# Kernel tuning notes

Measured on AMD Instinct MI355X. Metric: run time of the kernel, lower is better.

Reference implementation:

```python
import jax, jax.numpy as jnp
import numpy as np

D_MODEL = 1024
N_HEADS = 16
HEAD_DIM = D_MODEL // N_HEADS
FF_DIM = 1024  # repo bug: linear2 is Linear(d_model, ff_dim); ff_dim==d_model required for residual
EPS = 1e-5


def _linear_params(k, d_in, d_out):
    kw, kb = jax.random.split(k)
    bound = 1.0 / np.sqrt(d_in)
    W = jax.random.uniform(kw, (d_out, d_in), minval=-bound, maxval=bound, dtype=jnp.float32)
    b = jax.random.uniform(kb, (d_out,), minval=-bound, maxval=bound, dtype=jnp.float32)
    return W, b


def setup_inputs() -> dict:
    key = jax.random.key(0)
    ks = jax.random.split(key, 8)
    src = jax.random.normal(ks[0], (4, 2048, D_MODEL), dtype=jnp.float32)
    Wq, bq = _linear_params(ks[1], D_MODEL, D_MODEL)
    Wk, bk = _linear_params(ks[2], D_MODEL, D_MODEL)
    Wv, bv = _linear_params(ks[3], D_MODEL, D_MODEL)
    Wo, bo = _linear_params(ks[4], D_MODEL, D_MODEL)
    W1, b1 = _linear_params(ks[5], D_MODEL, FF_DIM)
    W2, b2 = _linear_params(ks[6], D_MODEL, FF_DIM)
    g1 = jnp.ones((D_MODEL,), jnp.float32); be1 = jnp.zeros((D_MODEL,), jnp.float32)
    g2 = jnp.ones((D_MODEL,), jnp.float32); be2 = jnp.zeros((D_MODEL,), jnp.float32)
    return {"src": src, "Wq": Wq, "bq": bq, "Wk": Wk, "bk": bk, "Wv": Wv, "bv": bv,
            "Wo": Wo, "bo": bo, "W1": W1, "b1": b1, "W2": W2, "b2": b2,
            "g1": g1, "be1": be1, "g2": g2, "be2": be2}


def _layernorm(x, g, b):
    mu = jnp.mean(x, axis=-1, keepdims=True)
    var = jnp.var(x, axis=-1, keepdims=True)
    return (x - mu) * jax.lax.rsqrt(var + EPS) * g + b


def _mha(x, Wq, bq, Wk, bk, Wv, bv, Wo, bo):
    B, S, _ = x.shape
    def proj(W, b):
        return (x @ W.T + b).reshape(B, S, N_HEADS, HEAD_DIM).transpose(0, 2, 1, 3)
    Q, K, V = proj(Wq, bq), proj(Wk, bk), proj(Wv, bv)
    scale = jnp.float32(np.sqrt(HEAD_DIM))
    energy = jnp.einsum('bhqd,bhkd->bhqk', Q, K) / scale
    attn = jax.nn.softmax(energy, axis=-1)
    out = jnp.einsum('bhqk,bhkd->bhqd', attn, V)
    out = out.transpose(0, 2, 1, 3).reshape(B, S, D_MODEL)
    return out @ Wo.T + bo


def reference(src, Wq, bq, Wk, bk, Wv, bv, Wo, bo, W1, b1, W2, b2, g1, be1, g2, be2):
    x = src
    x = x + _mha(_layernorm(x, g1, be1), Wq, bq, Wk, bk, Wv, bv, Wo, bo)
    h = _layernorm(x, g2, be2)
    ff = jax.nn.relu(h @ W1.T + b1) @ W2.T + b2
    return x + ff
```

## Files before the change

### kernel.cpp

```cpp
#include <hip/hip_runtime.h>
#include <stdint.h>

typedef __attribute__((ext_vector_type(8))) short    bf16x8;
typedef __attribute__((ext_vector_type(4))) short    bf16x4;
typedef __attribute__((ext_vector_type(4))) float    f32x4;
typedef __attribute__((ext_vector_type(8))) uint16_t u16x8;
typedef __attribute__((ext_vector_type(4))) uint16_t u16x4;

#define D_MODEL 1024
#define SEQ     2048
#define NB      4
#define NH      16
#define HD      64
#define MTOK    8192

__device__ __forceinline__ float bf2f(uint16_t u) {
    union { uint32_t i; float f; } x; x.i = ((uint32_t)u) << 16; return x.f;
}
__device__ __forceinline__ uint16_t f2bf(float f) {
    union { float f; uint32_t i; } x; x.f = f;
    uint32_t r = (x.i + 0x7fffu + ((x.i >> 16) & 1u)) >> 16;
    return (uint16_t)r;
}
__device__ __forceinline__ void gload16(const void* g, void* l) {
    __builtin_amdgcn_global_load_lds(
        (const __attribute__((address_space(1))) unsigned int*)g,
        (__attribute__((address_space(3))) unsigned int*)l, 16, 0, 0);
}
__device__ __forceinline__ bf16x8 lds_ld8(const uint16_t* p) {
    bf16x4 a = *(const bf16x4*)p;
    bf16x4 b = *(const bf16x4*)(p + 4);
    bf16x8 r;
    r[0] = a[0]; r[1] = a[1]; r[2] = a[2]; r[3] = a[3];
    r[4] = b[0]; r[5] = b[1]; r[6] = b[2]; r[7] = b[3];
    return r;
}
__device__ __forceinline__ uint32_t pk_bf16_trunc(float lo, float hi) {
    return __builtin_amdgcn_perm(__float_as_uint(hi), __float_as_uint(lo), 0x07060302u);
}

__global__ __launch_bounds__(256)
void cvt_all(const float* __restrict__ s0, const float* __restrict__ s1,
             const float* __restrict__ s2, const float* __restrict__ s3,
             const float* __restrict__ s4, const float* __restrict__ s5,
             uint16_t* __restrict__ dQKV, uint16_t* __restrict__ dWo,
             uint16_t* __restrict__ dW1, uint16_t* __restrict__ dW2)
{
    const float* srcs[6] = {s0, s1, s2, s3, s4, s5};
    uint16_t* dsts[6] = {dQKV, dQKV + (size_t)D_MODEL * D_MODEL,
                         dQKV + 2 * (size_t)D_MODEL * D_MODEL, dWo, dW1, dW2};
    const float* in = srcs[blockIdx.y];
    uint16_t* out = dsts[blockIdx.y];
    const int i = (blockIdx.x * 256 + threadIdx.x) * 4;
    float4 v = *(const float4*)(in + i);
    u16x4 o;
    o[0] = f2bf(v.x); o[1] = f2bf(v.y); o[2] = f2bf(v.z); o[3] = f2bf(v.w);
    *(u16x4*)(out + i) = o;
}

__global__ __launch_bounds__(256)
void ln_kernel(const float* __restrict__ x, const float* __restrict__ g,
               const float* __restrict__ be, uint16_t* __restrict__ y)
{
    const int row = blockIdx.x;
    const int tid = threadIdx.x;
    const size_t base = (size_t)row * D_MODEL + tid * 4;
    float4 v = *(const float4*)(x + base);
    float f[4] = {v.x, v.y, v.z, v.w};
    float sum = 0.f, sq = 0.f;
#pragma unroll
    for (int e = 0; e < 4; e++) { sum += f[e]; sq += f[e] * f[e]; }
#pragma unroll
    for (int o = 32; o > 0; o >>= 1) { sum += __shfl_down(sum, o); sq += __shfl_down(sq, o); }
    __shared__ float ps[4], pq[4];
    const int lane = tid & 63, wid = tid >> 6;
    if (lane == 0) { ps[wid] = sum; pq[wid] = sq; }
    __syncthreads();
    const float ts = ps[0] + ps[1] + ps[2] + ps[3];
    const float tq = pq[0] + pq[1] + pq[2] + pq[3];
    const float mean = ts * (1.0f / D_MODEL);
    const float var  = tq * (1.0f / D_MODEL) - mean * mean;
    const float rstd = rsqrtf(var + 1e-5f);
    float4 gv = *(const float4*)(g + tid * 4);
    float4 bv = *(const float4*)(be + tid * 4);
    const float gg[4] = {gv.x, gv.y, gv.z, gv.w};
    const float bb[4] = {bv.x, bv.y, bv.z, bv.w};
    u16x4 outv;
#pragma unroll
    for (int e = 0; e < 4; e++)
        outv[e] = f2bf((f[e] - mean) * rstd * gg[e] + bb[e]);
    *(u16x4*)(y + base) = outv;
}

template<int RESID, int RELU, int OUTF32>
__global__ __launch_bounds__(256, 4)
void gemm_bt64(const uint16_t* __restrict__ A, const uint16_t* __restrict__ W,
               const float* __restrict__ bias, const float* __restrict__ resid,
               void* __restrict__ Cv)
{
    __shared__ uint16_t lA[64 * 32];
    __shared__ uint16_t lB[128 * 32];
    const int tid  = threadIdx.x;
    const int lane = tid & 63;
    const int quad = lane >> 4;
    const int l16  = lane & 15;
    const int wid  = tid >> 6;
    const int wm   = wid >> 1;
    const int wn   = wid & 1;
    const int m0   = blockIdx.y * 64;
    const int n0   = blockIdx.x * 128;

    f32x4 acc[2][4];
#pragma unroll
    for (int i = 0; i < 2; i++)
#pragma unroll
        for (int j = 0; j < 4; j++) acc[i][j] = (f32x4){0.f, 0.f, 0.f, 0.f};

    const int sr = tid >> 2;
    const int sc = (tid & 3) * 8;
    const uint16_t* gA0 = A + (size_t)(m0 + sr) * D_MODEL + sc;
    const uint16_t* gW0 = W + (size_t)(n0 + sr) * D_MODEL + sc;
    const uint16_t* gW1 = gW0 + (size_t)64 * D_MODEL;
    uint16_t* sA0 = &lA[tid * 8];
    uint16_t* sB0 = &lB[tid * 8];
    uint16_t* sB1 = sB0 + 2048;

    for (int k0 = 0; k0 < D_MODEL; k0 += 32) {
        __syncthreads();
        gload16(gA0 + k0, sA0);
        gload16(gW0 + k0, sB0);
        gload16(gW1 + k0, sB1);
        __syncthreads();
        bf16x8 af[2], bfr[4];
#pragma unroll
        for (int i = 0; i < 2; i++)
            af[i] = *(const bf16x8*)&lA[(wm * 32 + i * 16 + l16) * 32 + quad * 8];
#pragma unroll
        for (int j = 0; j < 4; j++)
            bfr[j] = *(const bf16x8*)&lB[(wn * 64 + j * 16 + l16) * 32 + quad * 8];
#pragma unroll
        for (int i = 0; i < 2; i++)
#pragma unroll
            for (int j = 0; j < 4; j++)
                acc[i][j] = __builtin_amdgcn_mfma_f32_16x16x32_bf16(af[i], bfr[j], acc[i][j], 0, 0, 0);
    }

#pragma unroll
    for (int j = 0; j < 4; j++) {
        const int col = n0 + wn * 64 + j * 16 + l16;
        const float bv = bias[col];
#pragma unroll
        for (int i = 0; i < 2; i++) {
            const int row = m0 + wm * 32 + i * 16 + quad * 4;
#pragma unroll
            for (int r = 0; r < 4; r++) {
                float v = acc[i][j][r] + bv;
                const size_t idx = (size_t)(row + r) * D_MODEL + col;
                if (RESID) v += resid[idx];
                if (RELU)  v = fmaxf(v, 0.0f);
                if (OUTF32) ((float*)Cv)[idx] = v;
                else        ((uint16_t*)Cv)[idx] = f2bf(v);
            }
        }
    }
}

#define QSCALE 0.18033688f
__global__ __launch_bounds__(256, 3)
void gemm_qkv(const uint16_t* __restrict__ A, const uint16_t* __restrict__ Wqkv,
              const float* __restrict__ bq, const float* __restrict__ bk,
              const float* __restrict__ bv, uint16_t* __restrict__ Qb,
              uint16_t* __restrict__ Kb, uint16_t* __restrict__ Vt)
{
    __shared__ uint16_t lA[128 * 32];
    __shared__ uint16_t lB[128 * 32];
    const int tid  = threadIdx.x;
    const int lane = tid & 63;
    const int quad = lane >> 4;
    const int l16  = lane & 15;
    const int wid  = tid >> 6;
    const int wm   = wid >> 1;
    const int wn   = wid & 1;
    const int t0   = blockIdx.y * 128;
    const int n0   = blockIdx.x * 128;
    const int which = n0 >> 10;
    const int lc0   = n0 & 1023;

    f32x4 acc[4][4];
#pragma unroll
    for (int i = 0; i < 4; i++)
#pragma unroll
        for (int j = 0; j < 4; j++) acc[i][j] = (f32x4){0.f, 0.f, 0.f, 0.f};

    const int sr = tid >> 2;
    const int sc = (tid & 3) * 8;
    const uint16_t* gA0 = A + (size_t)(t0 + sr) * D_MODEL + sc;
    const uint16_t* gA1 = gA0 + (size_t)64 * D_MODEL;
    const uint16_t* gW0 = Wqkv + (size_t)(n0 + sr) * D_MODEL + sc;
    const uint16_t* gW1 = gW0 + (size_t)64 * D_MODEL;
    uint16_t* sA0 = &lA[tid * 8];
    uint16_t* sA1 = sA0 + 2048;
    uint16_t* sB0 = &lB[tid * 8];
    uint16_t* sB1 = sB0 + 2048;

    for (int k0 = 0; k0 < D_MODEL; k0 += 32) {
        __syncthreads();
        gload16(gA0 + k0, sA0);
        gload16(gA1 + k0, sA1);
        gload16(gW0 + k0, sB0);
        gload16(gW1 + k0, sB1);
        __syncthreads();
        bf16x8 fa[4], fb[4];
        if (which != 2) {
#pragma unroll
            for (int i = 0; i < 4; i++)
                fa[i] = *(const bf16x8*)&lA[(wm * 64 + i * 16 + l16) * 32 + quad * 8];
#pragma unroll
            for (int j = 0; j < 4; j++)
                fb[j] = *(const bf16x8*)&lB[(wn * 64 + j * 16 + l16) * 32 + quad * 8];
        } else {
#pragma unroll
            for (int i = 0; i < 4; i++)
                fa[i] = *(const bf16x8*)&lB[(wm * 64 + i * 16 + l16) * 32 + quad * 8];
#pragma unroll
            for (int j = 0; j < 4; j++)
                fb[j] = *(const bf16x8*)&lA[(wn * 64 + j * 16 + l16) * 32 + quad * 8];
        }
#pragma unroll
        for (int i = 0; i < 4; i++)
#pragma unroll
            for (int j = 0; j < 4; j++)
                acc[i][j] = __builtin_amdgcn_mfma_f32_16x16x32_bf16(fa[i], fb[j], acc[i][j], 0, 0, 0);
    }

    if (which != 2) {
        const float* bias = (which == 0) ? bq : bk;
        uint16_t* C = (which == 0) ? Qb : Kb;
        const float alpha = (which == 0) ? QSCALE : 1.0f;
#pragma unroll
        for (int j = 0; j < 4; j++) {
            const int col = lc0 + wn * 64 + j * 16 + l16;
            const float bvv = bias[col];
#pragma unroll
            for (int i = 0; i < 4; i++) {
                const int row = t0 + wm * 64 + i * 16 + quad * 4;
#pragma unroll
                for (int r = 0; r < 4; r++)
                    C[(size_t)(row + r) * D_MODEL + col] = f2bf((acc[i][j][r] + bvv) * alpha);
            }
        }
    } else {
#pragma unroll
        for (int i = 0; i < 4; i++) {
#pragma unroll
            for (int r = 0; r < 4; r++) {
                const int wrow = lc0 + wm * 64 + i * 16 + quad * 4 + r;
                const float bvv = bv[wrow];
#pragma unroll
                for (int j = 0; j < 4; j++) {
                    const int tok = t0 + wn * 64 + j * 16 + l16;
                    Vt[(size_t)wrow * MTOK + tok] = f2bf(acc[i][j][r] + bvv);
                }
            }
        }
    }
}

#define PST 68
__global__ __launch_bounds__(256, 4)
void attn_kernel(const uint16_t* __restrict__ Q, const uint16_t* __restrict__ K,
                 const uint16_t* __restrict__ Vt, uint16_t* __restrict__ O)
{
    __shared__ uint16_t sQP[128 * PST];
    __shared__ uint16_t sK [64 * PST];
    __shared__ uint16_t sVt[64 * PST];
    __shared__ float    sSt[128];

    const int tid  = threadIdx.x;
    const int lane = tid & 63;
    const int quad = lane >> 4;
    const int l16  = lane & 15;
    const int w    = tid >> 6;

    const int bh = blockIdx.x;
    const int h  = bh & (NH - 1);
    const int b  = bh >> 4;
    const int q0 = blockIdx.y * 128;
    const size_t headoff = (size_t)h * HD;
    const size_t bbase   = (size_t)b * SEQ;

    const int r8 = tid >> 3;
    const int c8 = (tid & 7) * 8;

#pragma unroll
    for (int i = 0; i < 4; i++)
        gload16(Q + (bbase + q0 + i * 32 + r8) * D_MODEL + headoff + c8, &sQP[i * 2048 + tid * 8]);
    __syncthreads();

    bf16x8 qa[2][2];
#pragma unroll
    for (int i = 0; i < 2; i++)
#pragma unroll
        for (int ks = 0; ks < 2; ks++)
            qa[i][ks] = *(const bf16x8*)&sQP[(w * 32 + i * 16 + l16) * 64 + ks * 32 + quad * 8];

    f32x4 oacc[2][4];
#pragma unroll
    for (int i = 0; i < 2; i++)
#pragma unroll
        for (int n = 0; n < 4; n++) oacc[i][n] = (f32x4){0.f, 0.f, 0.f, 0.f};
    float lrun[2] = {0.f, 0.f};

    const uint16_t* gK  = K  + bbase * D_MODEL + headoff;
    const uint16_t* gVt = Vt + headoff * MTOK + bbase;

    for (int kv0 = 0; kv0 < SEQ; kv0 += 64) {
        u16x8 kreg[2], vreg[2];
#pragma unroll
        for (int i = 0; i < 2; i++) {
            const int row = i * 32 + r8;
            kreg[i] = *(const u16x8*)(gK + (size_t)(kv0 + row) * D_MODEL + c8);
            vreg[i] = *(const u16x8*)(gVt + (size_t)row * MTOK + kv0 + c8);
        }
        __syncthreads();
#pragma unroll
        for (int i = 0; i < 2; i++) {
            const int row = i * 32 + r8;
            *(u16x4*)&sK [(size_t)row * PST + c8]     = (u16x4){kreg[i][0], kreg[i][1], kreg[i][2], kreg[i][3]};
            *(u16x4*)&sK [(size_t)row * PST + c8 + 4] = (u16x4){kreg[i][4], kreg[i][5], kreg[i][6], kreg[i][7]};
            *(u16x4*)&sVt[(size_t)row * PST + c8]     = (u16x4){vreg[i][0], vreg[i][1], vreg[i][2], vreg[i][3]};
            *(u16x4*)&sVt[(size_t)row * PST + c8 + 4] = (u16x4){vreg[i][4], vreg[i][5], vreg[i][6], vreg[i][7]};
        }
        __syncthreads();

        f32x4 st[4][2];
#pragma unroll
        for (int j = 0; j < 4; j++)
#pragma unroll
            for (int i = 0; i < 2; i++) st[j][i] = (f32x4){0.f, 0.f, 0.f, 0.f};
#pragma unroll
        for (int ks = 0; ks < 2; ks++)
#pragma unroll
            for (int j = 0; j < 4; j++) {
                bf16x8 kb = lds_ld8(&sK[(j * 16 + l16) * PST + ks * 32 + quad * 8]);
#pragma unroll
                for (int i = 0; i < 2; i++)
                    st[j][i] = __builtin_amdgcn_mfma_f32_16x16x32_bf16(kb, qa[i][ks], st[j][i], 0, 0, 0);
            }

#pragma unroll
        for (int i = 0; i < 2; i++) {
            float rs = 0.f;
#pragma unroll
            for (int j = 0; j < 4; j++) {
#pragma unroll
                for (int r = 0; r < 4; r++) {
                    const float p = __builtin_amdgcn_exp2f(st[j][i][r]);
                    st[j][i][r] = p;
                    rs += p;
                }
            }
            lrun[i] += rs;
#pragma unroll
            for (int j = 0; j < 4; j++) {
                uint2 pk;
                pk.x = pk_bf16_trunc(st[j][i][0], st[j][i][1]);
                pk.y = pk_bf16_trunc(st[j][i][2], st[j][i][3]);
                *(uint2*)&sQP[(size_t)(w * 32 + i * 16 + l16) * PST + j * 16 + quad * 4] = pk;
            }
        }

#pragma unroll
        for (int i = 0; i < 2; i++)
#pragma unroll
            for (int ks = 0; ks < 2; ks++) {
                bf16x8 pa = lds_ld8(&sQP[(size_t)(w * 32 + i * 16 + l16) * PST + ks * 32 + quad * 8]);
#pragma unroll
                for (int n = 0; n < 4; n++) {
                    bf16x8 vb = lds_ld8(&sVt[(n * 16 + l16) * PST + ks * 32 + quad * 8]);
                    oacc[i][n] = __builtin_amdgcn_mfma_f32_16x16x32_bf16(pa, vb, oacc[i][n], 0, 0, 0);
                }
            }
    }

#pragma unroll
    for (int i = 0; i < 2; i++) {
        lrun[i] += __shfl_xor(lrun[i], 16);
        lrun[i] += __shfl_xor(lrun[i], 32);
        sSt[w * 32 + i * 16 + l16] = 1.0f / lrun[i];
    }
#pragma unroll
    for (int i = 0; i < 2; i++)
#pragma unroll
        for (int r = 0; r < 4; r++) {
            const size_t row = bbase + q0 + w * 32 + i * 16 + quad * 4 + r;
            const float inv = sSt[w * 32 + i * 16 + quad * 4 + r];
#pragma unroll
            for (int n = 0; n < 4; n++)
                O[row * D_MODEL + headoff + n * 16 + l16] = f2bf(oacc[i][n][r] * inv);
        }
}

extern "C" void kernel_launch(void* const* d_in, const int* in_sizes, int n_in,
                              void* d_out, int out_size, void* d_ws, size_t ws_size,
                              hipStream_t stream)
{
    const float* src = (const float*)d_in[0];
    const float* Wq  = (const float*)d_in[1];
    const float* bq  = (const float*)d_in[2];
    const float* Wk  = (const float*)d_in[3];
    const float* bk  = (const float*)d_in[4];
    const float* Wv  = (const float*)d_in[5];
    const float* bv  = (const float*)d_in[6];
    const float* Wo  = (const float*)d_in[7];
    const float* bo  = (const float*)d_in[8];
    const float* W1  = (const float*)d_in[9];
    const float* b1  = (const float*)d_in[10];
    const float* W2  = (const float*)d_in[11];
    const float* b2  = (const float*)d_in[12];
    const float* g1  = (const float*)d_in[13];
    const float* be1 = (const float*)d_in[14];
    const float* g2  = (const float*)d_in[15];
    const float* be2 = (const float*)d_in[16];
    float* out = (float*)d_out;

    uint16_t* ws  = (uint16_t*)d_ws;
    const size_t BUF = (size_t)MTOK * D_MODEL;
    const size_t WSZ = (size_t)D_MODEL * D_MODEL;
    uint16_t* xn1  = ws;
    uint16_t* Vtb  = ws + BUF;
    uint16_t* wQKV = ws + 2 * BUF;
    uint16_t* wWo  = wQKV + 3 * WSZ;
    uint16_t* wW1  = wWo + WSZ;
    uint16_t* wW2  = wW1 + WSZ;
    uint16_t* Qb   = (uint16_t*)d_out;
    uint16_t* Kb   = Qb + BUF;
    float*    x2   = (float*)d_out;

    dim3 blk(256);
    cvt_all<<<dim3(1024, 6), 256, 0, stream>>>(Wq, Wk, Wv, Wo, W1, W2, wQKV, wWo, wW1, wW2);
    ln_kernel<<<8192, 256, 0, stream>>>(src, g1, be1, xn1);
    gemm_qkv<<<dim3(24, 64), blk, 0, stream>>>(xn1, wQKV, bq, bk, bv, Qb, Kb, Vtb);
    attn_kernel<<<dim3(64, 16), 256, 0, stream>>>(Qb, Kb, Vtb, xn1);
    gemm_bt64<1, 0, 1><<<dim3(8, 128), blk, 0, stream>>>(xn1, wWo, bo, src, x2);
    ln_kernel<<<8192, 256, 0, stream>>>(x2, g2, be2, xn1);
    gemm_bt64<0, 1, 0><<<dim3(8, 128), blk, 0, stream>>>(xn1, wW1, b1, nullptr, Vtb);
    gemm_bt64<1, 0, 1><<<dim3(8, 128), blk, 0, stream>>>(Vtb, wW2, b2, x2, out);
}
```

Measured before the change: 389.7 us.

## Enlarge GEMM tile to 128x128 and prefetch next K/V tile in attention

The three dense GEMMs move from 64x128 to 128x128 block tiles, so each wave computes a 64x64 sub-tile with 16 MFMAs per K-step. This raises reuse of LDS fragments per global load and halves the grid, at the cost of more accumulator registers and lower occupancy (launch bound 3). In the attention kernel, the global loads of the next K/V tile are issued into registers right after the LDS store barrier, so they overlap with the current tile's compute instead of stalling at the loop head.

```diff
diff --git a/kernel.cpp b/kernel.cpp
--- a/kernel.cpp
+++ b/kernel.cpp
@@ -93,12 +93,12 @@
 }
 
 template<int RESID, int RELU, int OUTF32>
-__global__ __launch_bounds__(256, 4)
-void gemm_bt64(const uint16_t* __restrict__ A, const uint16_t* __restrict__ W,
-               const float* __restrict__ bias, const float* __restrict__ resid,
-               void* __restrict__ Cv)
-{
-    __shared__ uint16_t lA[64 * 32];
+__global__ __launch_bounds__(256, 3)
+void gemm_bt128(const uint16_t* __restrict__ A, const uint16_t* __restrict__ W,
+                const float* __restrict__ bias, const float* __restrict__ resid,
+                void* __restrict__ Cv)
+{
+    __shared__ uint16_t lA[128 * 32];
     __shared__ uint16_t lB[128 * 32];
     const int tid  = threadIdx.x;
     const int lane = tid & 63;
@@ -107,54 +107,57 @@
     const int wid  = tid >> 6;
     const int wm   = wid >> 1;
     const int wn   = wid & 1;
-    const int m0   = blockIdx.y * 64;
+    const int m0   = blockIdx.y * 128;
     const int n0   = blockIdx.x * 128;
 
-    f32x4 acc[2][4];
-#pragma unroll
-    for (int i = 0; i < 2; i++)
+    f32x4 acc[4][4];
+#pragma unroll
+    for (int i = 0; i < 4; i++)
 #pragma unroll
         for (int j = 0; j < 4; j++) acc[i][j] = (f32x4){0.f, 0.f, 0.f, 0.f};
 
     const int sr = tid >> 2;
     const int sc = (tid & 3) * 8;
     const uint16_t* gA0 = A + (size_t)(m0 + sr) * D_MODEL + sc;
+    const uint16_t* gA1 = gA0 + (size_t)64 * D_MODEL;
     const uint16_t* gW0 = W + (size_t)(n0 + sr) * D_MODEL + sc;
     const uint16_t* gW1 = gW0 + (size_t)64 * D_MODEL;
     uint16_t* sA0 = &lA[tid * 8];
+    uint16_t* sA1 = sA0 + 2048;
     uint16_t* sB0 = &lB[tid * 8];
     uint16_t* sB1 = sB0 + 2048;
 
     for (int k0 = 0; k0 < D_MODEL; k0 += 32) {
         __syncthreads();
         gload16(gA0 + k0, sA0);
+        gload16(gA1 + k0, sA1);
         gload16(gW0 + k0, sB0);
         gload16(gW1 + k0, sB1);
         __syncthreads();
-        bf16x8 af[2], bfr[4];
-#pragma unroll
-        for (int i = 0; i < 2; i++)
-            af[i] = *(const bf16x8*)&lA[(wm * 32 + i * 16 + l16) * 32 + quad * 8];
+        bf16x8 fa[4], fb[4];
+#pragma unroll
+        for (int i = 0; i < 4; i++)
+            fa[i] = *(const bf16x8*)&lA[(wm * 64 + i * 16 + l16) * 32 + quad * 8];
 #pragma unroll
         for (int j = 0; j < 4; j++)
-            bfr[j] = *(const bf16x8*)&lB[(wn * 64 + j * 16 + l16) * 32 + quad * 8];
-#pragma unroll
-        for (int i = 0; i < 2; i++)
+            fb[j] = *(const bf16x8*)&lB[(wn * 64 + j * 16 + l16) * 32 + quad * 8];
+#pragma unroll
+        for (int i = 0; i < 4; i++)
 #pragma unroll
             for (int j = 0; j < 4; j++)
-                acc[i][j] = __builtin_amdgcn_mfma_f32_16x16x32_bf16(af[i], bfr[j], acc[i][j], 0, 0, 0);
+                acc[i][j] = __builtin_amdgcn_mfma_f32_16x16x32_bf16(fa[i], fb[j], acc[i][j], 0, 0, 0);
     }
 
 #pragma unroll
     for (int j = 0; j < 4; j++) {
         const int col = n0 + wn * 64 + j * 16 + l16;
-        const float bv = bias[col];
-#pragma unroll
-        for (int i = 0; i < 2; i++) {
-            const int row = m0 + wm * 32 + i * 16 + quad * 4;
+        const float bvv = bias[col];
+#pragma unroll
+        for (int i = 0; i < 4; i++) {
+            const int row = m0 + wm * 64 + i * 16 + quad * 4;
 #pragma unroll
             for (int r = 0; r < 4; r++) {
-                float v = acc[i][j][r] + bv;
+                float v = acc[i][j][r] + bvv;
                 const size_t idx = (size_t)(row + r) * D_MODEL + col;
                 if (RESID) v += resid[idx];
                 if (RELU)  v = fmaxf(v, 0.0f);
@@ -314,14 +317,15 @@
     const uint16_t* gK  = K  + bbase * D_MODEL + headoff;
     const uint16_t* gVt = Vt + headoff * MTOK + bbase;
 
+    u16x8 kreg[2], vreg[2];
+#pragma unroll
+    for (int i = 0; i < 2; i++) {
+        const int row = i * 32 + r8;
+        kreg[i] = *(const u16x8*)(gK + (size_t)row * D_MODEL + c8);
+        vreg[i] = *(const u16x8*)(gVt + (size_t)row * MTOK + c8);
+    }
+
     for (int kv0 = 0; kv0 < SEQ; kv0 += 64) {
-        u16x8 kreg[2], vreg[2];
-#pragma unroll
-        for (int i = 0; i < 2; i++) {
-            const int row = i * 32 + r8;
-            kreg[i] = *(const u16x8*)(gK + (size_t)(kv0 + row) * D_MODEL + c8);
-            vreg[i] = *(const u16x8*)(gVt + (size_t)row * MTOK + kv0 + c8);
-        }
         __syncthreads();
 #pragma unroll
         for (int i = 0; i < 2; i++) {
@@ -332,6 +336,16 @@
             *(u16x4*)&sVt[(size_t)row * PST + c8 + 4] = (u16x4){vreg[i][4], vreg[i][5], vreg[i][6], vreg[i][7]};
         }
         __syncthreads();
+
+        if (kv0 + 64 < SEQ) {
+            const int kvn = kv0 + 64;
+#pragma unroll
+            for (int i = 0; i < 2; i++) {
+                const int row = i * 32 + r8;
+                kreg[i] = *(const u16x8*)(gK + (size_t)(kvn + row) * D_MODEL + c8);
+                vreg[i] = *(const u16x8*)(gVt + (size_t)row * MTOK + kvn + c8);
+            }
+        }
 
         f32x4 st[4][2];
 #pragma unroll
@@ -442,8 +456,8 @@
     ln_kernel<<<8192, 256, 0, stream>>>(src, g1, be1, xn1);
     gemm_qkv<<<dim3(24, 64), blk, 0, stream>>>(xn1, wQKV, bq, bk, bv, Qb, Kb, Vtb);
     attn_kernel<<<dim3(64, 16), 256, 0, stream>>>(Qb, Kb, Vtb, xn1);
-    gemm_bt64<1, 0, 1><<<dim3(8, 128), blk, 0, stream>>>(xn1, wWo, bo, src, x2);
+    gemm_bt128<1, 0, 1><<<dim3(8, 64), blk, 0, stream>>>(xn1, wWo, bo, src, x2);
     ln_kernel<<<8192, 256, 0, stream>>>(x2, g2, be2, xn1);
-    gemm_bt64<0, 1, 0><<<dim3(8, 128), blk, 0, stream>>>(xn1, wW1, b1, nullptr, Vtb);
-    gemm_bt64<1, 0, 1><<<dim3(8, 128), blk, 0, stream>>>(Vtb, wW2, b2, x2, out);
-}
+    gemm_bt128<0, 1, 0><<<dim3(8, 64), blk, 0, stream>>>(xn1, wW1, b1, nullptr, Vtb);
+    gemm_bt128<1, 0, 1><<<dim3(8, 64), blk, 0, stream>>>(Vtb, wW2, b2, x2, out);
+}
```

Result: slower. 398.4 us (+2.2%).
